# Optimization experiments

Measured on AMD Instinct MI355X. Metric: run time of the kernel, lower is better.

## Reference

```python
import jax, jax.numpy as jnp
import numpy as np

D_MODEL = 1024
NUM_HEADS = 16
HEAD_DIM = D_MODEL // NUM_HEADS
THETA = 10000.0
B, S = 2, 2048


def _apply_rope(t, cos, sin):
    # t: [B, H, S, hd]; cos/sin: [S, hd//2]
    te = t[..., 0::2]
    to = t[..., 1::2]
    re = te * cos - to * sin
    ro = te * sin + to * cos
    out = jnp.stack([re, ro], axis=-1)  # [B,H,S,hd//2,2]
    return out.reshape(t.shape)


def setup_inputs() -> dict:
    key = jax.random.key(0)
    kx, kq, kk, kv, ko = jax.random.split(key, 5)
    std = 2.0 / (2 * D_MODEL) ** 0.5
    def w(k):
        return jnp.clip(std * jax.random.normal(k, (D_MODEL, D_MODEL), jnp.float32), -3.0 * std, 3.0 * std)
    return {
        "x": jax.random.normal(kx, (B, S, D_MODEL), jnp.float32),
        "Wq": w(kq),
        "Wk": w(kk),
        "Wv": w(kv),
        "Wo": w(ko),
    }


def reference(x, Wq, Wk, Wv, Wo):
    Bv, Sv, _ = x.shape
    def proj(W):
        return jnp.einsum('bsd,ed->bse', x, W).reshape(Bv, Sv, NUM_HEADS, HEAD_DIM).transpose(0, 2, 1, 3)
    q, k, v = proj(Wq), proj(Wk), proj(Wv)

    pos = jnp.arange(Sv, dtype=jnp.float32)
    inv_freq = THETA ** (-jnp.arange(0, HEAD_DIM, 2, dtype=jnp.float32) / HEAD_DIM)
    ang = pos[:, None] * inv_freq[None, :]  # [S, hd//2]
    cos, sin = jnp.cos(ang), jnp.sin(ang)
    q = _apply_rope(q, cos, sin)
    k = _apply_rope(k, cos, sin)

    scale = 1.0 / jnp.sqrt(jnp.float32(HEAD_DIM))
    scores = jnp.einsum('bhqd,bhkd->bhqk', q.astype(jnp.float32), k.astype(jnp.float32)) * scale
    causal = jnp.tril(jnp.ones((Sv, Sv), dtype=bool))
    scores = jnp.where(causal[None, None], scores, -jnp.inf)
    attn = jax.nn.softmax(scores, axis=-1)
    out = jnp.einsum('bhqk,bhkd->bhqd', attn, v.astype(jnp.float32))
    out = out.transpose(0, 2, 1, 3).reshape(Bv, Sv, D_MODEL)
    return jnp.einsum('bsd,ed->bse', out, Wo)
```

## Files before the change

kernel.cpp:

```cpp
#include <hip/hip_runtime.h>
#include <hip/hip_bf16.h>
#include <stdint.h>

typedef __bf16 bf16x8 __attribute__((ext_vector_type(8)));
typedef float  f32x4  __attribute__((ext_vector_type(4)));

__device__ __forceinline__ float bf2f(unsigned short u) {
    union { float f; uint32_t i; } v; v.i = ((uint32_t)u) << 16; return v.f;
}
__device__ __forceinline__ unsigned short f2bf(float f) {
    union { float f; uint32_t i; } v; v.f = f;
    uint32_t r = v.i + 0x7FFF + ((v.i >> 16) & 1);
    return (unsigned short)(r >> 16);
}

#define GLD_LDS(gptr, lptr) \
    __builtin_amdgcn_global_load_lds( \
        (const __attribute__((address_space(1))) void*)(gptr), \
        (__attribute__((address_space(3))) void*)(lptr), 16, 0, 0)

__global__ __launch_bounds__(256) void detect_dtype(
    const uint32_t* __restrict__ x, int* __restrict__ flag)
{
    __shared__ int cnt[256];
    int tid = threadIdx.x;
    uint32_t u = x[tid];
    int e = (u >> 7) & 0xFF;
    cnt[tid] = (e >= 100 && e <= 140) ? 1 : 0;
    __syncthreads();
    for (int s = 128; s > 0; s >>= 1) {
        if (tid < s) cnt[tid] += cnt[tid + s];
        __syncthreads();
    }
    if (tid == 0) flag[0] = (cnt[0] >= 128) ? 1 : 0;
}

__global__ __launch_bounds__(256) void convert_inputs(
    const void* __restrict__ x,  const void* __restrict__ wq,
    const void* __restrict__ wk, const void* __restrict__ wv,
    const void* __restrict__ wo, unsigned short* __restrict__ dst,
    unsigned short* __restrict__ wob_dst, const int* __restrict__ flag)
{
    int c = blockIdx.x * 256 + threadIdx.x;
    const int isf32 = (flag[0] == 0) ? 1 : 0;
    const void* src; size_t off; unsigned short* out;
    if (c < 524288)      { src = x;  off = (size_t)c * 8;            out = dst + (size_t)c * 8; }
    else if (c < 655360) { src = wq; off = (size_t)(c - 524288) * 8; out = dst + (size_t)c * 8; }
    else if (c < 786432) { src = wk; off = (size_t)(c - 655360) * 8; out = dst + (size_t)c * 8; }
    else if (c < 917504) { src = wv; off = (size_t)(c - 786432) * 8; out = dst + (size_t)c * 8; }
    else                 { src = wo; off = (size_t)(c - 917504) * 8; out = wob_dst + off; }
    unsigned short t[8];
    if (isf32) {
        const float* s = (const float*)src + off;
        float4 f0 = *(const float4*)s;
        float4 f1 = *(const float4*)(s + 4);
        t[0] = f2bf(f0.x); t[1] = f2bf(f0.y); t[2] = f2bf(f0.z); t[3] = f2bf(f0.w);
        t[4] = f2bf(f1.x); t[5] = f2bf(f1.y); t[6] = f2bf(f1.z); t[7] = f2bf(f1.w);
    } else {
        *(uint4*)t = *(const uint4*)((const unsigned short*)src + off);
    }
    *(uint4*)out = *(const uint4*)t;
}

__global__ __launch_bounds__(256) void gemm_bt(
    const unsigned short* __restrict__ A,
    const unsigned short* __restrict__ B0,
    const unsigned short* __restrict__ B1,
    const unsigned short* __restrict__ B2,
    void* __restrict__ O0,
    void* __restrict__ O1,
    void* __restrict__ O2,
    int mode, const int* __restrict__ flag)
{
    const int K = 1024;
    __shared__ __align__(16) unsigned short As[128 * 64];
    __shared__ __align__(16) unsigned short Bs[128 * 64];

    const int isf32 = (flag[0] == 0) ? 1 : 0;

    const int tid  = threadIdx.x;
    const int lane = tid & 63;
    const int wid  = tid >> 6;
    const int wm   = wid >> 1;
    const int wn   = wid & 1;
    const int lr   = lane & 15;
    const int quad = lane >> 4;
    const int q8   = quad * 8;

    const int m0  = blockIdx.y * 128;
    const int n0g = blockIdx.x * 128;
    const int sel = n0g >> 10;
    const unsigned short* B = (sel == 0) ? B0 : ((sel == 1) ? B1 : B2);
    void* Optr              = (sel == 0) ? O0 : ((sel == 1) ? O1 : O2);
    const int n0  = n0g & 1023;

    f32x4 acc[4][4] = {};

    for (int kk = 0; kk < K; kk += 64) {
        __syncthreads();
        for (int p = 0; p < 4; ++p) {
            int c   = p * 256 + tid;
            int row = c >> 3;
            int c8  = (c & 7) * 8;
            GLD_LDS(&A[(size_t)(m0 + row) * K + kk + c8], &As[c * 8]);
            GLD_LDS(&B[(size_t)(n0 + row) * K + kk + c8], &Bs[c * 8]);
        }
        __syncthreads();

        for (int ks = 0; ks < 64; ks += 32) {
            bf16x8 af[4], bf[4];
            for (int t = 0; t < 4; ++t) {
                af[t] = *(const bf16x8*)&As[(wm * 64 + t * 16 + lr) * 64 + ks + q8];
                bf[t] = *(const bf16x8*)&Bs[(wn * 64 + t * 16 + lr) * 64 + ks + q8];
            }
            for (int mt = 0; mt < 4; ++mt)
                for (int nt = 0; nt < 4; ++nt)
                    acc[mt][nt] = __builtin_amdgcn_mfma_f32_16x16x32_bf16(
                        af[mt], bf[nt], acc[mt][nt], 0, 0, 0);
        }
    }

    for (int mt = 0; mt < 4; ++mt) {
        for (int nt = 0; nt < 4; ++nt) {
            for (int r = 0; r < 4; ++r) {
                int m  = m0 + wm * 64 + mt * 16 + quad * 4 + r;
                int nl = n0 + wn * 64 + nt * 16 + lr;
                float val = acc[mt][nt][r];
                if (mode == 0) {
                    if (isf32) ((float*)Optr)[(size_t)m * 1024 + nl] = val;
                    else ((unsigned short*)Optr)[(size_t)m * 1024 + nl] = f2bf(val);
                } else {
                    int b = m >> 11, s = m & 2047;
                    int h = nl >> 6, d = nl & 63;
                    ((unsigned short*)Optr)[((size_t)(b * 16 + h) * 2048 + s) * 64 + d] = f2bf(val);
                }
            }
        }
    }
}

__global__ __launch_bounds__(256) void transpose_v(
    const unsigned short* __restrict__ V,
    unsigned short* __restrict__ Vt)
{
    __shared__ unsigned short T[64 * 65];
    const int tid = threadIdx.x;
    const int s0  = blockIdx.x * 64;
    const int bh  = blockIdx.y;

    const unsigned short* src = V + ((size_t)bh * 2048 + s0) * 64;
    for (int p = 0; p < 2; ++p) {
        int c = p * 256 + tid;
        int s  = c >> 3;
        int d8 = (c & 7) * 8;
        uint4 raw = *(const uint4*)&src[s * 64 + d8];
        unsigned short t[8];
        *(uint4*)t = raw;
        for (int j = 0; j < 8; ++j) T[s * 65 + d8 + j] = t[j];
    }
    __syncthreads();
    unsigned short* dst = Vt + (size_t)bh * 64 * 2048 + s0;
    for (int p = 0; p < 2; ++p) {
        int c = p * 256 + tid;
        int d  = c >> 3;
        int s8 = (c & 7) * 8;
        unsigned short t[8];
        for (int j = 0; j < 8; ++j) t[j] = T[(s8 + j) * 65 + d];
        *(uint4*)&dst[(size_t)d * 2048 + s8] = *(const uint4*)t;
    }
}

__global__ __launch_bounds__(256) void rope_kernel(
    unsigned short* __restrict__ Q, unsigned short* __restrict__ Kp)
{
    const int CH = 32 * 2048 * 8;
    int idx = blockIdx.x * 256 + threadIdx.x;
    bool isK = idx >= CH;
    int j = isK ? (idx - CH) : idx;
    unsigned short* p = isK ? Kp : Q;

    int c8   = j & 7;
    int srow = j >> 3;
    int s    = srow & 2047;
    int off  = srow * 64 + c8 * 8;

    uint4 raw = *(const uint4*)&p[off];
    unsigned short t[8];
    *(uint4*)t = raw;
    float sf = (float)s;
    float qs = isK ? 1.0f : 0.125f;
    for (int jj = 0; jj < 4; ++jj) {
        int i = c8 * 4 + jj;
        float inv = __expf(-0.2878231366f * (float)i);
        float ang = sf * inv;
        float sn = __sinf(ang);
        float cs = __cosf(ang);
        float e = bf2f(t[2 * jj]);
        float o = bf2f(t[2 * jj + 1]);
        t[2 * jj]     = f2bf((e * cs - o * sn) * qs);
        t[2 * jj + 1] = f2bf((e * sn + o * cs) * qs);
    }
    *(uint4*)&p[off] = *(const uint4*)t;
}

__global__ __launch_bounds__(256) void attn_kernel(
    const unsigned short* __restrict__ Q,
    const unsigned short* __restrict__ Kp,
    const unsigned short* __restrict__ Vt,
    unsigned short* __restrict__ P0,
    unsigned short* __restrict__ P1,
    float* __restrict__ Lsum)
{
    __shared__ __align__(16) unsigned short Ks[2][4096];
    __shared__ __align__(16) unsigned short Vs[2][4096];
    __shared__ __align__(16) unsigned short Ps[4 * 32 * 68];

    const int tid  = threadIdx.x;
    const int lane = tid & 63;
    const int w    = tid >> 6;
    const int lr   = lane & 15;
    const int quad = lane >> 4;
    const int q8   = quad * 8;
    const int wps  = w * 2176;

    const int bh    = blockIdx.x;
    const int y     = blockIdx.y;
    const int split = y >> 4;
    const int yq    = y & 15;
    const int qb    = (yq < 8) ? yq : (23 - yq);
    const int q0    = qb * 128;
    const int kb0   = split ? (qb + 1) : 0;
    const int kb1   = split ? (2 * qb + 1) : qb;

    unsigned short* Pout = split ? P1 : P0;

    const unsigned short* KbBase = Kp + (size_t)bh * 2048 * 64;
    const unsigned short* VbBase = Vt + (size_t)bh * 131072;

    auto stage = [&](int kb, int buf) {
        const unsigned short* Kb = KbBase + kb * 64 * 64;
        const unsigned short* Vb = VbBase + kb * 64;
        for (int p = 0; p < 2; ++p) {
            int c    = p * 256 + tid;
            int f    = c >> 6, l = c & 63;
            int nt   = f >> 1, ks = f & 1;
            int lr_s = l & 15, qd = l >> 4;
            GLD_LDS(&Kb[(nt * 16 + lr_s) * 64 + ks * 32 + qd * 8], &Ks[buf][c * 8]);
            GLD_LDS(&Vb[(size_t)(nt * 16 + lr_s) * 2048 + ks * 32 + qd * 8], &Vs[buf][c * 8]);
        }
    };

    bf16x8 qa[2][2];
    for (int mt = 0; mt < 2; ++mt) {
        const unsigned short* Qw = Q + ((size_t)bh * 2048 + q0 + mt * 64 + w * 16 + lr) * 64;
        qa[mt][0] = *(const bf16x8*)&Qw[q8];
        qa[mt][1] = *(const bf16x8*)&Qw[32 + q8];
    }

    stage(kb0, 0);

    f32x4 oacc[2][4] = {};
    float lpart[2][4] = {};
    const int l8 = lane * 8;

    for (int kb = kb0; kb <= kb1; ++kb) {
        const int cur = (kb - kb0) & 1;
        __syncthreads();
        if (kb < kb1) stage(kb + 1, cur ^ 1);

        f32x4 sacc[2][4] = {};
        for (int nt = 0; nt < 4; ++nt) {
            bf16x8 kf0 = *(const bf16x8*)&Ks[cur][(nt * 2 + 0) * 512 + l8];
            bf16x8 kf1 = *(const bf16x8*)&Ks[cur][(nt * 2 + 1) * 512 + l8];
            for (int mt = 0; mt < 2; ++mt) {
                sacc[mt][nt] = __builtin_amdgcn_mfma_f32_16x16x32_bf16(qa[mt][0], kf0, sacc[mt][nt], 0, 0, 0);
                sacc[mt][nt] = __builtin_amdgcn_mfma_f32_16x16x32_bf16(qa[mt][1], kf1, sacc[mt][nt], 0, 0, 0);
            }
        }

        if (kb >= 2 * qb) {
            for (int mt = 0; mt < 2; ++mt) {
                int rowb = q0 + mt * 64 + w * 16 + quad * 4;
                for (int nt = 0; nt < 4; ++nt) {
                    int col = kb * 64 + nt * 16 + lr;
                    for (int r = 0; r < 4; ++r)
                        if (col > rowb + r) sacc[mt][nt][r] = -3.0e38f;
                }
            }
        }

        for (int mt = 0; mt < 2; ++mt) {
            int pbase = wps + mt * 1088;
            for (int r = 0; r < 4; ++r) {
                for (int nt = 0; nt < 4; ++nt) {
                    float pv = __expf(sacc[mt][nt][r] - 16.0f);
                    lpart[mt][r] += pv;
                    Ps[pbase + (quad * 4 + r) * 68 + nt * 16 + lr] = f2bf(pv);
                }
            }
        }

        for (int ks = 0; ks < 2; ++ks) {
            bf16x8 pa0 = *(const bf16x8*)&Ps[wps + lr * 68 + ks * 32 + q8];
            bf16x8 pa1 = *(const bf16x8*)&Ps[wps + 1088 + lr * 68 + ks * 32 + q8];
            for (int nt = 0; nt < 4; ++nt) {
                bf16x8 vf = *(const bf16x8*)&Vs[cur][(nt * 2 + ks) * 512 + l8];
                oacc[0][nt] = __builtin_amdgcn_mfma_f32_16x16x32_bf16(pa0, vf, oacc[0][nt], 0, 0, 0);
                oacc[1][nt] = __builtin_amdgcn_mfma_f32_16x16x32_bf16(pa1, vf, oacc[1][nt], 0, 0, 0);
            }
        }
    }

    for (int mt = 0; mt < 2; ++mt) {
        for (int r = 0; r < 4; ++r) {
            float l = lpart[mt][r];
            for (int off = 1; off < 16; off <<= 1)
                l += __shfl_xor(l, off, 64);
            int s = q0 + mt * 64 + w * 16 + quad * 4 + r;
            for (int nt = 0; nt < 4; ++nt)
                Pout[((size_t)bh * 2048 + s) * 64 + nt * 16 + lr] = f2bf(oacc[mt][nt][r]);
            if (lr == 0) Lsum[split * 65536 + bh * 2048 + s] = l;
        }
    }
}

__global__ __launch_bounds__(256) void combine_kernel(
    const unsigned short* __restrict__ P0,
    const unsigned short* __restrict__ P1,
    const float* __restrict__ Lsum,
    unsigned short* __restrict__ AO)
{
    int c = blockIdx.x * 256 + threadIdx.x;
    int row = c >> 3;
    int d0  = (c & 7) * 8;
    int bh  = row >> 11, s = row & 2047;
    int b   = bh >> 4, h = bh & 15;

    float inv = 1.0f / (Lsum[row] + Lsum[65536 + row]);
    unsigned short a[8], bb[8], o[8];
    *(uint4*)a  = *(const uint4*)&P0[(size_t)c * 8];
    *(uint4*)bb = *(const uint4*)&P1[(size_t)c * 8];
    for (int j = 0; j < 8; ++j)
        o[j] = f2bf((bf2f(a[j]) + bf2f(bb[j])) * inv);
    *(uint4*)&AO[((size_t)b * 2048 + s) * 1024 + h * 64 + d0] = *(const uint4*)o;
}

extern "C" void kernel_launch(void* const* d_in, const int* in_sizes, int n_in,
                              void* d_out, int out_size, void* d_ws, size_t ws_size,
                              hipStream_t stream)
{
    const void* x  = d_in[0];
    const void* Wq = d_in[1];
    const void* Wk = d_in[2];
    const void* Wv = d_in[3];
    const void* Wo = d_in[4];

    int* flag = (int*)d_ws;
    unsigned short* base = (unsigned short*)d_ws + 8;
    const size_t M1 = 1048576;
    unsigned short* xb  = base;
    unsigned short* wqb = base + 4 * M1;
    unsigned short* wkb = base + 5 * M1;
    unsigned short* wvb = base + 6 * M1;
    unsigned short* q   = base + 8 * M1;
    unsigned short* k   = base + 12 * M1;
    unsigned short* v   = base + 16 * M1;
    unsigned short* wob = base + 20 * M1;
    float*          Ls  = (float*)(base + 21 * M1);
    unsigned short* vt  = xb;
    unsigned short* P0  = v;
    unsigned short* P1  = wqb;
    unsigned short* aof = k;

    detect_dtype<<<dim3(1), 256, 0, stream>>>((const uint32_t*)x, flag);
    convert_inputs<<<dim3(4096), 256, 0, stream>>>(x, Wq, Wk, Wv, Wo, base, wob, flag);
    gemm_bt<<<dim3(24, 32), 256, 0, stream>>>(xb, wqb, wkb, wvb, q, k, v, 1, flag);
    rope_kernel<<<dim3(4096), 256, 0, stream>>>(q, k);
    transpose_v<<<dim3(32, 32), 256, 0, stream>>>(v, vt);
    attn_kernel<<<dim3(32, 32), 256, 0, stream>>>(q, k, vt, P0, P1, Ls);
    combine_kernel<<<dim3(4096), 256, 0, stream>>>(P0, P1, Ls, aof);
    gemm_bt<<<dim3(8, 32), 256, 0, stream>>>(aof, wob, wob, wob, d_out, d_out, d_out, 0, flag);
}
```

Before: 243.0 us.

## Fuse RoPE into QKV GEMM epilogue, merge dtype detect, restructure P staging

Applies RoPE and the Q scaling inside the QKV projection GEMM epilogue, using a lane shuffle to fetch the even/odd partner, and removes the separate rope kernel pass over Q and K. Dtype detection moves into every convert block, so each block computes the flag redundantly and one kernel launch is dropped. The attention kernel's P tile in LDS is re-laid out to match the MFMA A-fragment so each lane reads it with one contiguous load, and LDS use shrinks. The PV product is now interleaved per m-tile. Risks: the shuffle pairing relies on the accumulator lane layout, and the extra sin/cos work lands in the GEMM epilogue.

```diff
diff --git a/kernel.cpp b/kernel.cpp
--- a/kernel.cpp
+++ b/kernel.cpp
@@ -19,12 +19,15 @@
         (const __attribute__((address_space(1))) void*)(gptr), \
         (__attribute__((address_space(3))) void*)(lptr), 16, 0, 0)
 
-__global__ __launch_bounds__(256) void detect_dtype(
-    const uint32_t* __restrict__ x, int* __restrict__ flag)
+__global__ __launch_bounds__(256) void convert_inputs(
+    const void* __restrict__ x,  const void* __restrict__ wq,
+    const void* __restrict__ wk, const void* __restrict__ wv,
+    const void* __restrict__ wo, unsigned short* __restrict__ dst,
+    unsigned short* __restrict__ wob_dst, int* __restrict__ flag)
 {
     __shared__ int cnt[256];
-    int tid = threadIdx.x;
-    uint32_t u = x[tid];
+    const int tid = threadIdx.x;
+    uint32_t u = ((const uint32_t*)x)[tid];
     int e = (u >> 7) & 0xFF;
     cnt[tid] = (e >= 100 && e <= 140) ? 1 : 0;
     __syncthreads();
@@ -32,17 +35,10 @@
         if (tid < s) cnt[tid] += cnt[tid + s];
         __syncthreads();
     }
-    if (tid == 0) flag[0] = (cnt[0] >= 128) ? 1 : 0;
-}
-
-__global__ __launch_bounds__(256) void convert_inputs(
-    const void* __restrict__ x,  const void* __restrict__ wq,
-    const void* __restrict__ wk, const void* __restrict__ wv,
-    const void* __restrict__ wo, unsigned short* __restrict__ dst,
-    unsigned short* __restrict__ wob_dst, const int* __restrict__ flag)
-{
-    int c = blockIdx.x * 256 + threadIdx.x;
-    const int isf32 = (flag[0] == 0) ? 1 : 0;
+    const int isf32 = (cnt[0] >= 128) ? 0 : 1;
+    if (blockIdx.x == 0 && tid == 0) flag[0] = isf32 ? 0 : 1;
+
+    int c = blockIdx.x * 256 + tid;
     const void* src; size_t off; unsigned short* out;
     if (c < 524288)      { src = x;  off = (size_t)c * 8;            out = dst + (size_t)c * 8; }
     else if (c < 655360) { src = wq; off = (size_t)(c - 524288) * 8; out = dst + (size_t)c * 8; }
@@ -132,6 +128,15 @@
                 } else {
                     int b = m >> 11, s = m & 2047;
                     int h = nl >> 6, d = nl & 63;
+                    if (sel < 2) {
+                        float partner = __shfl_xor(val, 1, 64);
+                        float inv = __expf(-0.2878231366f * (float)(d >> 1));
+                        float ang = (float)s * inv;
+                        float sn = __sinf(ang), cs = __cosf(ang);
+                        val = (d & 1) ? (partner * sn + val * cs)
+                                      : (val * cs - partner * sn);
+                        if (sel == 0) val *= 0.125f;
+                    }
                     ((unsigned short*)Optr)[((size_t)(b * 16 + h) * 2048 + s) * 64 + d] = f2bf(val);
                 }
             }
@@ -170,39 +175,6 @@
     }
 }
 
-__global__ __launch_bounds__(256) void rope_kernel(
-    unsigned short* __restrict__ Q, unsigned short* __restrict__ Kp)
-{
-    const int CH = 32 * 2048 * 8;
-    int idx = blockIdx.x * 256 + threadIdx.x;
-    bool isK = idx >= CH;
-    int j = isK ? (idx - CH) : idx;
-    unsigned short* p = isK ? Kp : Q;
-
-    int c8   = j & 7;
-    int srow = j >> 3;
-    int s    = srow & 2047;
-    int off  = srow * 64 + c8 * 8;
-
-    uint4 raw = *(const uint4*)&p[off];
-    unsigned short t[8];
-    *(uint4*)t = raw;
-    float sf = (float)s;
-    float qs = isK ? 1.0f : 0.125f;
-    for (int jj = 0; jj < 4; ++jj) {
-        int i = c8 * 4 + jj;
-        float inv = __expf(-0.2878231366f * (float)i);
-        float ang = sf * inv;
-        float sn = __sinf(ang);
-        float cs = __cosf(ang);
-        float e = bf2f(t[2 * jj]);
-        float o = bf2f(t[2 * jj + 1]);
-        t[2 * jj]     = f2bf((e * cs - o * sn) * qs);
-        t[2 * jj + 1] = f2bf((e * sn + o * cs) * qs);
-    }
-    *(uint4*)&p[off] = *(const uint4*)t;
-}
-
 __global__ __launch_bounds__(256) void attn_kernel(
     const unsigned short* __restrict__ Q,
     const unsigned short* __restrict__ Kp,
@@ -213,7 +185,7 @@
 {
     __shared__ __align__(16) unsigned short Ks[2][4096];
     __shared__ __align__(16) unsigned short Vs[2][4096];
-    __shared__ __align__(16) unsigned short Ps[4 * 32 * 68];
+    __shared__ __align__(16) unsigned short Ps[4096];
 
     const int tid  = threadIdx.x;
     const int lane = tid & 63;
@@ -221,7 +193,7 @@
     const int lr   = lane & 15;
     const int quad = lane >> 4;
     const int q8   = quad * 8;
-    const int wps  = w * 2176;
+    const int wps  = w * 1024;
 
     const int bh    = blockIdx.x;
     const int y     = blockIdx.y;
@@ -262,6 +234,8 @@
     f32x4 oacc[2][4] = {};
     float lpart[2][4] = {};
     const int l8 = lane * 8;
+    const int lr7 = lr & 7;
+    const int lrh = lr >> 3;
 
     for (int kb = kb0; kb <= kb1; ++kb) {
         const int cur = (kb - kb0) & 1;
@@ -290,23 +264,21 @@
         }
 
         for (int mt = 0; mt < 2; ++mt) {
-            int pbase = wps + mt * 1088;
             for (int r = 0; r < 4; ++r) {
                 for (int nt = 0; nt < 4; ++nt) {
                     float pv = __expf(sacc[mt][nt][r] - 16.0f);
                     lpart[mt][r] += pv;
-                    Ps[pbase + (quad * 4 + r) * 68 + nt * 16 + lr] = f2bf(pv);
+                    int ks = nt >> 1;
+                    int qr = (nt * 2 + lrh) & 3;
+                    Ps[wps + ks * 512 + (qr * 16 + quad * 4 + r) * 8 + lr7] = f2bf(pv);
                 }
             }
-        }
-
-        for (int ks = 0; ks < 2; ++ks) {
-            bf16x8 pa0 = *(const bf16x8*)&Ps[wps + lr * 68 + ks * 32 + q8];
-            bf16x8 pa1 = *(const bf16x8*)&Ps[wps + 1088 + lr * 68 + ks * 32 + q8];
-            for (int nt = 0; nt < 4; ++nt) {
-                bf16x8 vf = *(const bf16x8*)&Vs[cur][(nt * 2 + ks) * 512 + l8];
-                oacc[0][nt] = __builtin_amdgcn_mfma_f32_16x16x32_bf16(pa0, vf, oacc[0][nt], 0, 0, 0);
-                oacc[1][nt] = __builtin_amdgcn_mfma_f32_16x16x32_bf16(pa1, vf, oacc[1][nt], 0, 0, 0);
+            for (int ks = 0; ks < 2; ++ks) {
+                bf16x8 pa = *(const bf16x8*)&Ps[wps + ks * 512 + l8];
+                for (int nt = 0; nt < 4; ++nt) {
+                    bf16x8 vf = *(const bf16x8*)&Vs[cur][(nt * 2 + ks) * 512 + l8];
+                    oacc[mt][nt] = __builtin_amdgcn_mfma_f32_16x16x32_bf16(pa, vf, oacc[mt][nt], 0, 0, 0);
+                }
             }
         }
     }
@@ -372,10 +344,8 @@
     unsigned short* P1  = wqb;
     unsigned short* aof = k;
 
-    detect_dtype<<<dim3(1), 256, 0, stream>>>((const uint32_t*)x, flag);
     convert_inputs<<<dim3(4096), 256, 0, stream>>>(x, Wq, Wk, Wv, Wo, base, wob, flag);
     gemm_bt<<<dim3(24, 32), 256, 0, stream>>>(xb, wqb, wkb, wvb, q, k, v, 1, flag);
-    rope_kernel<<<dim3(4096), 256, 0, stream>>>(q, k);
     transpose_v<<<dim3(32, 32), 256, 0, stream>>>(v, vt);
     attn_kernel<<<dim3(32, 32), 256, 0, stream>>>(q, k, vt, P0, P1, Ls);
     combine_kernel<<<dim3(4096), 256, 0, stream>>>(P0, P1, Ls, aof);
```

Result: slower. 587.4 us (+141.7%).
